# Optimization experiments

Measured on AMD Instinct MI355X. Metric: run time of the kernel, lower is better.

The kernel has to match this reference:

```python
import jax, jax.numpy as jnp
import numpy as np

# Module hyperparameters (from init_kwargs)
LEARNING_RATE = 0.01  # not used inside compute_weight_update
TAU_PLUS = 20.0
TAU_MINUS = 20.0
A_PLUS = 0.005
A_MINUS = 0.00525
TARGET_RATE = 0.1
HOMEOSTATIC_RATE = 0.001
TAU_HOMEOSTATIC = 1000.0

B, T, N_PRE, N_POST = 16, 8192, 128, 128


def setup_inputs() -> dict:
    key = jax.random.key(0)
    k1, k2, k3 = jax.random.split(key, 3)
    # Bernoulli spike trains at ~target_rate firing probability
    pre_spikes = (jax.random.uniform(k1, (B, T, N_PRE)) < TARGET_RATE).astype(jnp.float32)
    post_spikes = (jax.random.uniform(k2, (B, T, N_POST)) < TARGET_RATE).astype(jnp.float32)
    weights = jax.random.uniform(k3, (N_PRE, N_POST), dtype=jnp.float32)
    return {"pre_spikes": pre_spikes, "post_spikes": post_spikes, "weights": weights, "dt": 1}


def _temporal_corr(x, kernel, pad):
    """Correlate x [B,T,N] along time with 1-D kernel [L], padding pad=(lo,hi)."""
    b, t, n = x.shape
    xr = jnp.moveaxis(x, 1, 2).reshape(b * n, 1, t)  # [B*N, 1, T]
    k = kernel.reshape(1, 1, -1).astype(x.dtype)
    y = jax.lax.conv_general_dilated(
        xr, k, window_strides=(1,), padding=[pad],
        dimension_numbers=("NCH", "OIH", "NCH"))
    return jnp.moveaxis(y.reshape(b, n, t), 2, 1)  # [B,T,N]


def reference(pre_spikes, post_spikes, weights, dt):
    b, t, n_pre = pre_spikes.shape
    dt = float(dt)

    # Homeostatic rate tracking (first call: avg rates initialized to target_rate)
    alpha = dt / TAU_HOMEOSTATIC
    current_post_rate = post_spikes.mean(axis=(0, 1))
    avg_post_rate = (1.0 - alpha) * TARGET_RATE + alpha * current_post_rate

    # Truncated exponential STDP window: tau in 1..min(int(3*tau)-1, ...) = 1..59
    L = int(TAU_PLUS * 3)  # 60 taps (tau=0 tap zeroed)
    taus = jnp.arange(L, dtype=jnp.float32)
    w_plus = jnp.where(taus > 0, A_PLUS * jnp.exp(-taus * dt / TAU_PLUS), 0.0)
    w_minus = jnp.where(taus > 0, A_MINUS * jnp.exp(-taus * dt / TAU_MINUS), 0.0)

    # LTP: post_filt[t] = sum_{tau>=1} w_plus[tau] * post[t+tau] (future, zero-padded)
    post_filt = _temporal_corr(post_spikes, w_plus, (0, L - 1))
    # LTD: pre_filt[t] = sum_{tau>=1} w_minus[tau] * pre[t-tau] (past, zero-padded)
    pre_filt = _temporal_corr(pre_spikes, w_minus[::-1], (L - 1, 0))

    # sum_t mean_b outer(pre[t], post_filt[t]) - outer(pre_filt[t], post[t]), then /T
    ltp = jnp.einsum("btp,btq->pq", pre_spikes, post_filt)
    ltd = jnp.einsum("btp,btq->pq", pre_filt, post_spikes)
    stdp_update = (ltp - ltd) / (b * t)

    # Homeostatic regulation pulls post rate toward target
    post_rate_error = avg_post_rate - TARGET_RATE
    homeostatic_update = -HOMEOSTATIC_RATE * post_rate_error[None, :] * weights

    return stdp_update + homeostatic_update
```

## Files before the change

### kernel.cpp

```cpp
#include <hip/hip_runtime.h>

#define BB 16
#define TT 8192
#define NN 128
constexpr int CHUNK = 256;
constexpr int NBLK  = BB * TT / CHUNK;
constexpr int OUTN  = NN * NN;
constexpr int GS    = 264;
constexpr int SLOTS = OUTN / 2;
constexpr int PROWS = 315;

typedef _Float16 f16x8 __attribute__((ext_vector_type(8)));
typedef _Float16 f16x2 __attribute__((ext_vector_type(2)));
typedef float    f32x4 __attribute__((ext_vector_type(4)));

__device__ __forceinline__ unsigned short h16(float x) {
    _Float16 h = (_Float16)x;
    return __builtin_bit_cast(unsigned short, h);
}
__device__ __forceinline__ unsigned int pack2(float x, float y) {
    return (unsigned int)h16(x) | ((unsigned int)h16(y) << 16);
}
__device__ __forceinline__ float2 ldL(const unsigned short* p_lds, int m, int q0) {
    const unsigned int v = *(const unsigned int*)&p_lds[m * NN + q0];
    const f16x2 h = __builtin_bit_cast(f16x2, v);
    return make_float2((float)h[0], (float)h[1]);
}

template<bool ATOMIC>
__global__ __launch_bounds__(512, 4)
void stdp_main(const float* __restrict__ pre, const float* __restrict__ post,
               const int* __restrict__ dtp,
               unsigned int* __restrict__ part, float* __restrict__ wpost,
               float* __restrict__ outat)
{
    __shared__ __align__(16) char smem[PROWS * NN * 2];
    unsigned short* post_lds = (unsigned short*)smem;
    unsigned short* g_lds    = (unsigned short*)smem;
    float*          lds_ps   = (float*)(smem + NN * GS * 2);

    const int tid   = threadIdx.x;
    const int blk   = blockIdx.x;
    const int b     = blk >> 5;
    const int chunk = blk & 31;
    const int t0    = chunk * CHUNK;
    const int wv    = tid >> 6;
    const int lane  = tid & 63;

    const float dtf = (float)(*dtp);
    const float r   = expf(-dtf * (1.0f / 20.0f));

    const float* pb = post + (size_t)b * TT * NN;
    const float* ab = pre  + (size_t)b * TT * NN;

    {
        const int c  = tid & 31;
        const int mr = tid >> 5;
        for (int m = mr; m < PROWS; m += 16) {
            const int t = t0 + 1 + m;
            float4 v = make_float4(0.f, 0.f, 0.f, 0.f);
            if (t < TT) v = *(const float4*)(pb + (size_t)t * NN + c * 4);
            *(uint2*)&post_lds[m * NN + c * 4] = make_uint2(pack2(v.x, v.y), pack2(v.z, v.w));
        }
    }
    __syncthreads();

    const int win  = wv;
    const int q0   = lane * 2;
    const int base = win * 32;
    float ps0 = 0.f, ps1 = 0.f;

    unsigned int pk0[16], pk1[16];
    {
        float2 p  = ldL(post_lds, base + 31, q0);
        float wt  = r;
        float gx = r * p.x, gy = r * p.y;
        ps0 += p.x; ps1 += p.y;
        #pragma unroll
        for (int tau = 2; tau <= 59; ++tau) {
            wt *= r;
            p = ldL(post_lds, base + 30 + tau, q0);
            gx = fmaf(wt, p.x, gx);
            gy = fmaf(wt, p.y, gy);
        }
        const float r60 = wt * r;
        pk0[15] = (unsigned int)h16(gx) << 16;
        pk1[15] = (unsigned int)h16(gy) << 16;
        #pragma unroll
        for (int c = 30; c >= 0; --c) {
            const float2 p1  = ldL(post_lds, base + c,      q0);
            const float2 p60 = ldL(post_lds, base + c + 59, q0);
            gx = r * (gx + p1.x) - r60 * p60.x;
            gy = r * (gy + p1.y) - r60 * p60.y;
            ps0 += p1.x; ps1 += p1.y;
            if (c & 1) {
                pk0[c >> 1] = (unsigned int)h16(gx) << 16;
                pk1[c >> 1] = (unsigned int)h16(gy) << 16;
            } else {
                pk0[c >> 1] |= h16(gx);
                pk1[c >> 1] |= h16(gy);
            }
        }
    }
    __syncthreads();

    {
        unsigned short* d0 = &g_lds[q0 * GS + win * 32];
        unsigned short* d1 = &g_lds[(q0 + 1) * GS + win * 32];
        #pragma unroll
        for (int s = 0; s < 4; ++s) {
            *(uint4*)(d0 + 8 * s) = make_uint4(pk0[4*s], pk0[4*s+1], pk0[4*s+2], pk0[4*s+3]);
            *(uint4*)(d1 + 8 * s) = make_uint4(pk1[4*s], pk1[4*s+1], pk1[4*s+2], pk1[4*s+3]);
        }
        lds_ps[win * NN + q0]     = ps0;
        lds_ps[win * NN + q0 + 1] = ps1;
    }
    __syncthreads();

    const int pr0 = wv * 16;
    f32x4 acc[8];
    #pragma unroll
    for (int qt = 0; qt < 8; ++qt) acc[qt] = (f32x4){0.f, 0.f, 0.f, 0.f};

    const float* abase = ab + (size_t)(t0 + (lane >> 4) * 8) * NN + pr0 + (lane & 15);
    float an[8];
    #pragma unroll
    for (int j = 0; j < 8; ++j) an[j] = abase[(size_t)j * NN];

    #pragma unroll
    for (int ks = 0; ks < 8; ++ks) {
        f16x8 af;
        #pragma unroll
        for (int j = 0; j < 8; ++j) af[j] = (_Float16)an[j];
        if (ks < 7) {
            const float* src = abase + (size_t)((ks + 1) * 32) * NN;
            #pragma unroll
            for (int j = 0; j < 8; ++j) an[j] = src[(size_t)j * NN];
        }
        const int koff = ks * 32 + (lane >> 4) * 8;
        #pragma unroll
        for (int qt = 0; qt < 8; ++qt) {
            const f16x8 bf = *(const f16x8*)&g_lds[(qt * 16 + (lane & 15)) * GS + koff];
            acc[qt] = __builtin_amdgcn_mfma_f32_16x16x32_f16(af, bf, acc[qt], 0, 0, 0);
        }
    }

    if constexpr (!ATOMIC) {
        unsigned int* dst = part + ((size_t)blk * 8 + wv) * 1024 + lane;
        #pragma unroll
        for (int qt = 0; qt < 8; ++qt)
            #pragma unroll
            for (int rp = 0; rp < 2; ++rp)
                dst[qt * 128 + rp * 64] = pack2(acc[qt][2 * rp], acc[qt][2 * rp + 1]);
    } else {
        #pragma unroll
        for (int qt = 0; qt < 8; ++qt)
            #pragma unroll
            for (int rg = 0; rg < 4; ++rg) {
                const int prow = pr0 + (lane >> 4) * 4 + rg;
                const int qcol = qt * 16 + (lane & 15);
                atomicAdd(&outat[prow * NN + qcol], acc[qt][rg]);
            }
    }

    __syncthreads();
    if (tid < NN) {
        float s = 0.f;
        #pragma unroll
        for (int w = 0; w < 8; ++w) s += lds_ps[w * NN + tid];
        if (chunk == 0) s += pb[tid];
        if constexpr (ATOMIC) atomicAdd(&wpost[tid], s);
        else wpost[(size_t)tid * NBLK + blk] = s;
    }
}

__global__ void hfac_kernel(const float* __restrict__ wpost, const int* __restrict__ dtp,
                            float* __restrict__ hfac, int nb)
{
    const int q = blockIdx.x;
    float s = 0.f;
    for (int k = threadIdx.x; k < nb; k += 64) s += wpost[(size_t)q * nb + k];
    #pragma unroll
    for (int off = 32; off; off >>= 1) s += __shfl_down(s, off, 64);
    if (threadIdx.x == 0) {
        const float dtf   = (float)(*dtp);
        const float alpha = dtf * 1e-3f;
        const float mean  = s * (1.0f / (float)(BB * TT));
        hfac[q] = -0.001f * (alpha * (mean - 0.1f));
    }
}

__global__ __launch_bounds__(512)
void finalize_ws(const unsigned int* __restrict__ part, const float* __restrict__ hfac,
                 const float* __restrict__ W, float* __restrict__ out)
{
    __shared__ float2 red[512];
    const int s    = threadIdx.x & 63;
    const int kq   = threadIdx.x >> 6;
    const int slot = blockIdx.x * 64 + s;
    float sx = 0.f, sy = 0.f;
    #pragma unroll 8
    for (int k = kq * 64; k < kq * 64 + 64; ++k) {
        const unsigned int v = part[(size_t)k * SLOTS + slot];
        const f16x2 h = __builtin_bit_cast(f16x2, v);
        sx += (float)h[0];
        sy += (float)h[1];
    }
    red[threadIdx.x] = make_float2(sx, sy);
    __syncthreads();
    if (threadIdx.x < 64) {
        #pragma unroll
        for (int g = 1; g < 8; ++g) {
            const float2 v = red[g * 64 + s];
            sx += v.x; sy += v.y;
        }
        sx += red[s].x - red[s].x + 0.f;
        float rx = red[s].x, ry = red[s].y;
        sx = sx - (sx - sx);
        float tx = rx, ty = ry;
        #pragma unroll
        for (int g = 1; g < 8; ++g) {
            const float2 v = red[g * 64 + s];
            tx += v.x; ty += v.y;
        }
        const int lane = slot & 63;
        const int rp   = (slot >> 6) & 1;
        const int qt   = (slot >> 7) & 7;
        const int wv   = slot >> 10;
        const int p    = wv * 16 + ((lane >> 4) << 2) + rp * 2;
        const int q    = qt * 16 + (lane & 15);
        const float scale = (float)((0.005 - 0.00525) / (double)(BB * TT));
        const float hf = hfac[q];
        out[p * NN + q]       = fmaf(tx, scale, hf * W[p * NN + q]);
        out[(p + 1) * NN + q] = fmaf(ty, scale, hf * W[(p + 1) * NN + q]);
    }
}

__global__ void finalize_at(const float* __restrict__ hfac, const float* __restrict__ W,
                            float* __restrict__ out)
{
    const int i = (blockIdx.x * 256 + threadIdx.x) * 2;
    const int q = i & 127;
    const float scale = (float)((0.005 - 0.00525) / (double)(BB * TT));
    float2 s = *(const float2*)(out + i);
    float2 w = *(const float2*)(W + i);
    float2 o;
    o.x = fmaf(s.x, scale, hfac[q] * w.x);
    o.y = fmaf(s.y, scale, hfac[q + 1] * w.y);
    *(float2*)(out + i) = o;
}

extern "C" void kernel_launch(void* const* d_in, const int* in_sizes, int n_in,
                              void* d_out, int out_size, void* d_ws, size_t ws_size,
                              hipStream_t stream)
{
    const float* pre  = (const float*)d_in[0];
    const float* post = (const float*)d_in[1];
    const float* W    = (const float*)d_in[2];
    const int*   dtp  = (const int*)d_in[3];
    float* out = (float*)d_out;

    const size_t part_bytes  = (size_t)NBLK * SLOTS * sizeof(unsigned int);
    const size_t wpost_bytes = (size_t)NBLK * NN * sizeof(float);
    const size_t need = part_bytes + wpost_bytes + NN * sizeof(float);

    if (ws_size >= need) {
        unsigned int* part = (unsigned int*)d_ws;
        float* wpost       = (float*)((char*)d_ws + part_bytes);
        float* hfac        = (float*)((char*)d_ws + part_bytes + wpost_bytes);
        hipLaunchKernelGGL((stdp_main<false>), dim3(NBLK), dim3(512), 0, stream,
                           pre, post, dtp, part, wpost, (float*)nullptr);
        hipLaunchKernelGGL(hfac_kernel, dim3(NN), dim3(64), 0, stream, wpost, dtp, hfac, NBLK);
        hipLaunchKernelGGL(finalize_ws, dim3(SLOTS / 64), dim3(512), 0, stream, part, hfac, W, out);
    } else {
        float* wpost = (float*)d_ws;
        float* hfac  = wpost + NN;
        hipMemsetAsync(d_out, 0, OUTN * sizeof(float), stream);
        hipMemsetAsync(wpost, 0, NN * sizeof(float), stream);
        hipLaunchKernelGGL((stdp_main<true>), dim3(NBLK), dim3(512), 0, stream,
                           pre, post, dtp, (unsigned int*)nullptr, wpost, out);
        hipLaunchKernelGGL(hfac_kernel, dim3(NN), dim3(64), 0, stream, wpost, dtp, hfac, 1);
        hipLaunchKernelGGL(finalize_at, dim3(OUTN / 512), dim3(256), 0, stream, hfac, W, out);
    }
}
```

Measured before the change: 164.7 us.

## Bit-pack post spikes via ballot, halve block size, fold hfac into finalize

Post spikes are packed into bitmasks with wave ballots and stored in LDS as bits instead of fp16. This shrinks shared memory and relies on the inputs being exactly 0/1. The main kernel drops to 256 threads, each wave computing two 16-row tiles in two time halves. The per-column post-spike sums now go to global atomics, which lets the hfac kernel be removed and its computation folded into finalize. The changes aim to cut LDS footprint and one launch, at the cost of atomics and bit-extract ALU work in the filter loop.

```diff
diff --git a/kernel.cpp b/kernel.cpp
--- a/kernel.cpp
+++ b/kernel.cpp
@@ -6,7 +6,7 @@
 constexpr int CHUNK = 256;
 constexpr int NBLK  = BB * TT / CHUNK;
 constexpr int OUTN  = NN * NN;
-constexpr int GS    = 264;
+constexpr int GS2   = 136;
 constexpr int SLOTS = OUTN / 2;
 constexpr int PROWS = 315;
 
@@ -21,23 +21,16 @@
 __device__ __forceinline__ unsigned int pack2(float x, float y) {
     return (unsigned int)h16(x) | ((unsigned int)h16(y) << 16);
 }
-__device__ __forceinline__ float2 ldL(const unsigned short* p_lds, int m, int q0) {
-    const unsigned int v = *(const unsigned int*)&p_lds[m * NN + q0];
-    const f16x2 h = __builtin_bit_cast(f16x2, v);
-    return make_float2((float)h[0], (float)h[1]);
-}
 
 template<bool ATOMIC>
-__global__ __launch_bounds__(512, 4)
+__global__ __launch_bounds__(256, 4)
 void stdp_main(const float* __restrict__ pre, const float* __restrict__ post,
                const int* __restrict__ dtp,
                unsigned int* __restrict__ part, float* __restrict__ wpost,
                float* __restrict__ outat)
 {
-    __shared__ __align__(16) char smem[PROWS * NN * 2];
-    unsigned short* post_lds = (unsigned short*)smem;
-    unsigned short* g_lds    = (unsigned short*)smem;
-    float*          lds_ps   = (float*)(smem + NN * GS * 2);
+    __shared__ __align__(16) unsigned int   bits_s[PROWS * 4];
+    __shared__ __align__(16) unsigned short g_s[NN * GS2];
 
     const int tid   = threadIdx.x;
     const int blk   = blockIdx.x;
@@ -53,146 +46,150 @@
     const float* pb = post + (size_t)b * TT * NN;
     const float* ab = pre  + (size_t)b * TT * NN;
 
-    {
-        const int c  = tid & 31;
-        const int mr = tid >> 5;
-        for (int m = mr; m < PROWS; m += 16) {
-            const int t = t0 + 1 + m;
-            float4 v = make_float4(0.f, 0.f, 0.f, 0.f);
-            if (t < TT) v = *(const float4*)(pb + (size_t)t * NN + c * 4);
-            *(uint2*)&post_lds[m * NN + c * 4] = make_uint2(pack2(v.x, v.y), pack2(v.z, v.w));
+    for (int it = 0; it < 40; ++it) {
+        const int half = lane >> 5;
+        const int m    = it * 8 + wv * 2 + half;
+        const int t    = t0 + 1 + m;
+        const int c4   = (lane & 31) * 4;
+        float4 v = make_float4(0.f, 0.f, 0.f, 0.f);
+        if (m < PROWS && t < TT) v = *(const float4*)(pb + (size_t)t * NN + c4);
+        const unsigned long long bx = __ballot(v.x != 0.0f);
+        const unsigned long long by = __ballot(v.y != 0.0f);
+        const unsigned long long bz = __ballot(v.z != 0.0f);
+        const unsigned long long bw = __ballot(v.w != 0.0f);
+        if (m < PROWS && (lane & 31) == 0) {
+            const int sh = half * 32;
+            *(uint4*)&bits_s[m * 4] = make_uint4(
+                (unsigned int)(bx >> sh), (unsigned int)(by >> sh),
+                (unsigned int)(bz >> sh), (unsigned int)(bw >> sh));
         }
     }
     __syncthreads();
 
-    const int win  = wv;
-    const int q0   = lane * 2;
-    const int base = win * 32;
+    const int q0 = lane * 2;
+    const int q1 = q0 + 1;
+    const int c0 = q0 & 3;
+    const int jb = q0 >> 2;
     float ps0 = 0.f, ps1 = 0.f;
 
-    unsigned int pk0[16], pk1[16];
-    {
-        float2 p  = ldL(post_lds, base + 31, q0);
-        float wt  = r;
-        float gx = r * p.x, gy = r * p.y;
-        ps0 += p.x; ps1 += p.y;
-        #pragma unroll
-        for (int tau = 2; tau <= 59; ++tau) {
-            wt *= r;
-            p = ldL(post_lds, base + 30 + tau, q0);
-            gx = fmaf(wt, p.x, gx);
-            gy = fmaf(wt, p.y, gy);
-        }
-        const float r60 = wt * r;
-        pk0[15] = (unsigned int)h16(gx) << 16;
-        pk1[15] = (unsigned int)h16(gy) << 16;
-        #pragma unroll
-        for (int c = 30; c >= 0; --c) {
-            const float2 p1  = ldL(post_lds, base + c,      q0);
-            const float2 p60 = ldL(post_lds, base + c + 59, q0);
-            gx = r * (gx + p1.x) - r60 * p60.x;
-            gy = r * (gy + p1.y) - r60 * p60.y;
-            ps0 += p1.x; ps1 += p1.y;
-            if (c & 1) {
-                pk0[c >> 1] = (unsigned int)h16(gx) << 16;
-                pk1[c >> 1] = (unsigned int)h16(gy) << 16;
-            } else {
-                pk0[c >> 1] |= h16(gx);
-                pk1[c >> 1] |= h16(gy);
-            }
-        }
-    }
-    __syncthreads();
-
-    {
-        unsigned short* d0 = &g_lds[q0 * GS + win * 32];
-        unsigned short* d1 = &g_lds[(q0 + 1) * GS + win * 32];
-        #pragma unroll
-        for (int s = 0; s < 4; ++s) {
-            *(uint4*)(d0 + 8 * s) = make_uint4(pk0[4*s], pk0[4*s+1], pk0[4*s+2], pk0[4*s+3]);
-            *(uint4*)(d1 + 8 * s) = make_uint4(pk1[4*s], pk1[4*s+1], pk1[4*s+2], pk1[4*s+3]);
-        }
-        lds_ps[win * NN + q0]     = ps0;
-        lds_ps[win * NN + q0 + 1] = ps1;
-    }
-    __syncthreads();
-
-    const int pr0 = wv * 16;
-    f32x4 acc[8];
+    f32x4 acc[2][8];
     #pragma unroll
-    for (int qt = 0; qt < 8; ++qt) acc[qt] = (f32x4){0.f, 0.f, 0.f, 0.f};
-
-    const float* abase = ab + (size_t)(t0 + (lane >> 4) * 8) * NN + pr0 + (lane & 15);
-    float an[8];
-    #pragma unroll
-    for (int j = 0; j < 8; ++j) an[j] = abase[(size_t)j * NN];
-
-    #pragma unroll
-    for (int ks = 0; ks < 8; ++ks) {
-        f16x8 af;
-        #pragma unroll
-        for (int j = 0; j < 8; ++j) af[j] = (_Float16)an[j];
-        if (ks < 7) {
-            const float* src = abase + (size_t)((ks + 1) * 32) * NN;
-            #pragma unroll
-            for (int j = 0; j < 8; ++j) an[j] = src[(size_t)j * NN];
-        }
-        const int koff = ks * 32 + (lane >> 4) * 8;
-        #pragma unroll
-        for (int qt = 0; qt < 8; ++qt) {
-            const f16x8 bf = *(const f16x8*)&g_lds[(qt * 16 + (lane & 15)) * GS + koff];
-            acc[qt] = __builtin_amdgcn_mfma_f32_16x16x32_f16(af, bf, acc[qt], 0, 0, 0);
-        }
-    }
+    for (int i = 0; i < 2; ++i)
+        #pragma unroll
+        for (int qt = 0; qt < 8; ++qt) acc[i][qt] = (f32x4){0.f, 0.f, 0.f, 0.f};
+
+    const int pr0 = wv * 32;
+
+    #pragma unroll 1
+    for (int s = 0; s < 2; ++s) {
+        const int mb = (s * 4 + wv) * 32;
+        unsigned int pk0[16], pk1[16];
+        {
+            #define RDP(mrow, px, py) {                                   \
+                const uint4 w4 = *(const uint4*)&bits_s[(mrow) * 4];      \
+                const unsigned int w0 = (c0 & 2) ? w4.z : w4.x;           \
+                const unsigned int w1 = (c0 & 2) ? w4.w : w4.y;           \
+                px = (float)((w0 >> jb) & 1u);                            \
+                py = (float)((w1 >> jb) & 1u);                            \
+            }
+            float px, py;
+            RDP(mb + 31, px, py);
+            float wt = r;
+            float gx = r * px, gy = r * py;
+            ps0 += px; ps1 += py;
+            #pragma unroll
+            for (int tau = 2; tau <= 59; ++tau) {
+                wt *= r;
+                RDP(mb + 30 + tau, px, py);
+                gx = fmaf(wt, px, gx);
+                gy = fmaf(wt, py, gy);
+            }
+            const float r60 = wt * r;
+            pk0[15] = (unsigned int)h16(gx) << 16;
+            pk1[15] = (unsigned int)h16(gy) << 16;
+            #pragma unroll
+            for (int c = 30; c >= 0; --c) {
+                float p1x, p1y, p60x, p60y;
+                RDP(mb + c,      p1x,  p1y);
+                RDP(mb + c + 59, p60x, p60y);
+                gx = r * (gx + p1x) - r60 * p60x;
+                gy = r * (gy + p1y) - r60 * p60y;
+                ps0 += p1x; ps1 += p1y;
+                if (c & 1) {
+                    pk0[c >> 1] = (unsigned int)h16(gx) << 16;
+                    pk1[c >> 1] = (unsigned int)h16(gy) << 16;
+                } else {
+                    pk0[c >> 1] |= h16(gx);
+                    pk1[c >> 1] |= h16(gy);
+                }
+            }
+            #undef RDP
+        }
+        if (s == 1) __syncthreads();
+        {
+            unsigned short* d0 = &g_s[q0 * GS2 + wv * 32];
+            unsigned short* d1 = &g_s[q1 * GS2 + wv * 32];
+            #pragma unroll
+            for (int k = 0; k < 4; ++k) {
+                *(uint4*)(d0 + 8 * k) = make_uint4(pk0[4*k], pk0[4*k+1], pk0[4*k+2], pk0[4*k+3]);
+                *(uint4*)(d1 + 8 * k) = make_uint4(pk1[4*k], pk1[4*k+1], pk1[4*k+2], pk1[4*k+3]);
+            }
+        }
+        __syncthreads();
+
+        #pragma unroll
+        for (int ks = 0; ks < 4; ++ks) {
+            const int trow = t0 + s * 128 + ks * 32 + (lane >> 4) * 8;
+            f16x8 af[2];
+            #pragma unroll
+            for (int i = 0; i < 2; ++i) {
+                const float* src = ab + (size_t)trow * NN + pr0 + i * 16 + (lane & 15);
+                #pragma unroll
+                for (int j = 0; j < 8; ++j)
+                    af[i][j] = (_Float16)src[(size_t)j * NN];
+            }
+            const int koff = ks * 32 + (lane >> 4) * 8;
+            #pragma unroll
+            for (int qt = 0; qt < 8; ++qt) {
+                const f16x8 bf = *(const f16x8*)&g_s[(qt * 16 + (lane & 15)) * GS2 + koff];
+                acc[0][qt] = __builtin_amdgcn_mfma_f32_16x16x32_f16(af[0], bf, acc[0][qt], 0, 0, 0);
+                acc[1][qt] = __builtin_amdgcn_mfma_f32_16x16x32_f16(af[1], bf, acc[1][qt], 0, 0, 0);
+            }
+        }
+    }
+
+    atomicAdd(&wpost[q0], ps0);
+    atomicAdd(&wpost[q1], ps1);
+    if (chunk == 0 && tid < NN) atomicAdd(&wpost[tid], pb[tid]);
 
     if constexpr (!ATOMIC) {
-        unsigned int* dst = part + ((size_t)blk * 8 + wv) * 1024 + lane;
-        #pragma unroll
-        for (int qt = 0; qt < 8; ++qt)
-            #pragma unroll
-            for (int rp = 0; rp < 2; ++rp)
-                dst[qt * 128 + rp * 64] = pack2(acc[qt][2 * rp], acc[qt][2 * rp + 1]);
+        unsigned int* dst = part + (size_t)blk * SLOTS + wv * 2048 + lane;
+        #pragma unroll
+        for (int i = 0; i < 2; ++i)
+            #pragma unroll
+            for (int qt = 0; qt < 8; ++qt)
+                #pragma unroll
+                for (int rp = 0; rp < 2; ++rp)
+                    dst[i * 1024 + qt * 128 + rp * 64] =
+                        pack2(acc[i][qt][2 * rp], acc[i][qt][2 * rp + 1]);
     } else {
         #pragma unroll
-        for (int qt = 0; qt < 8; ++qt)
-            #pragma unroll
-            for (int rg = 0; rg < 4; ++rg) {
-                const int prow = pr0 + (lane >> 4) * 4 + rg;
-                const int qcol = qt * 16 + (lane & 15);
-                atomicAdd(&outat[prow * NN + qcol], acc[qt][rg]);
-            }
-    }
-
-    __syncthreads();
-    if (tid < NN) {
-        float s = 0.f;
-        #pragma unroll
-        for (int w = 0; w < 8; ++w) s += lds_ps[w * NN + tid];
-        if (chunk == 0) s += pb[tid];
-        if constexpr (ATOMIC) atomicAdd(&wpost[tid], s);
-        else wpost[(size_t)tid * NBLK + blk] = s;
-    }
-}
-
-__global__ void hfac_kernel(const float* __restrict__ wpost, const int* __restrict__ dtp,
-                            float* __restrict__ hfac, int nb)
-{
-    const int q = blockIdx.x;
-    float s = 0.f;
-    for (int k = threadIdx.x; k < nb; k += 64) s += wpost[(size_t)q * nb + k];
-    #pragma unroll
-    for (int off = 32; off; off >>= 1) s += __shfl_down(s, off, 64);
-    if (threadIdx.x == 0) {
-        const float dtf   = (float)(*dtp);
-        const float alpha = dtf * 1e-3f;
-        const float mean  = s * (1.0f / (float)(BB * TT));
-        hfac[q] = -0.001f * (alpha * (mean - 0.1f));
+        for (int i = 0; i < 2; ++i)
+            #pragma unroll
+            for (int qt = 0; qt < 8; ++qt)
+                #pragma unroll
+                for (int rg = 0; rg < 4; ++rg) {
+                    const int prow = pr0 + i * 16 + (lane >> 4) * 4 + rg;
+                    const int qcol = qt * 16 + (lane & 15);
+                    atomicAdd(&outat[prow * NN + qcol], acc[i][qt][rg]);
+                }
     }
 }
 
 __global__ __launch_bounds__(512)
-void finalize_ws(const unsigned int* __restrict__ part, const float* __restrict__ hfac,
-                 const float* __restrict__ W, float* __restrict__ out)
+void finalize_ws(const unsigned int* __restrict__ part, const float* __restrict__ wpost,
+                 const int* __restrict__ dtp, const float* __restrict__ W,
+                 float* __restrict__ out)
 {
     __shared__ float2 red[512];
     const int s    = threadIdx.x & 63;
@@ -209,15 +206,7 @@
     red[threadIdx.x] = make_float2(sx, sy);
     __syncthreads();
     if (threadIdx.x < 64) {
-        #pragma unroll
-        for (int g = 1; g < 8; ++g) {
-            const float2 v = red[g * 64 + s];
-            sx += v.x; sy += v.y;
-        }
-        sx += red[s].x - red[s].x + 0.f;
-        float rx = red[s].x, ry = red[s].y;
-        sx = sx - (sx - sx);
-        float tx = rx, ty = ry;
+        float tx = red[s].x, ty = red[s].y;
         #pragma unroll
         for (int g = 1; g < 8; ++g) {
             const float2 v = red[g * 64 + s];
@@ -226,27 +215,34 @@
         const int lane = slot & 63;
         const int rp   = (slot >> 6) & 1;
         const int qt   = (slot >> 7) & 7;
-        const int wv   = slot >> 10;
-        const int p    = wv * 16 + ((lane >> 4) << 2) + rp * 2;
+        const int ii   = (slot >> 10) & 1;
+        const int wv   = slot >> 11;
+        const int p    = wv * 32 + ii * 16 + ((lane >> 4) << 2) + rp * 2;
         const int q    = qt * 16 + (lane & 15);
         const float scale = (float)((0.005 - 0.00525) / (double)(BB * TT));
-        const float hf = hfac[q];
+        const float dtf   = (float)(*dtp);
+        const float alpha = dtf * 1e-3f;
+        const float hf    = -0.001f * (alpha * (wpost[q] * (1.0f / (BB * TT)) - 0.1f));
         out[p * NN + q]       = fmaf(tx, scale, hf * W[p * NN + q]);
         out[(p + 1) * NN + q] = fmaf(ty, scale, hf * W[(p + 1) * NN + q]);
     }
 }
 
-__global__ void finalize_at(const float* __restrict__ hfac, const float* __restrict__ W,
-                            float* __restrict__ out)
+__global__ void finalize_at(const float* __restrict__ wpost, const int* __restrict__ dtp,
+                            const float* __restrict__ W, float* __restrict__ out)
 {
     const int i = (blockIdx.x * 256 + threadIdx.x) * 2;
     const int q = i & 127;
     const float scale = (float)((0.005 - 0.00525) / (double)(BB * TT));
-    float2 s = *(const float2*)(out + i);
-    float2 w = *(const float2*)(W + i);
+    const float dtf   = (float)(*dtp);
+    const float alpha = dtf * 1e-3f;
+    const float hf0   = -0.001f * (alpha * (wpost[q]     * (1.0f / (BB * TT)) - 0.1f));
+    const float hf1   = -0.001f * (alpha * (wpost[q + 1] * (1.0f / (BB * TT)) - 0.1f));
+    float2 sv = *(const float2*)(out + i);
+    float2 w  = *(const float2*)(W + i);
     float2 o;
-    o.x = fmaf(s.x, scale, hfac[q] * w.x);
-    o.y = fmaf(s.y, scale, hfac[q + 1] * w.y);
+    o.x = fmaf(sv.x, scale, hf0 * w.x);
+    o.y = fmaf(sv.y, scale, hf1 * w.y);
     *(float2*)(out + i) = o;
 }
 
@@ -260,26 +256,24 @@
     const int*   dtp  = (const int*)d_in[3];
     float* out = (float*)d_out;
 
-    const size_t part_bytes  = (size_t)NBLK * SLOTS * sizeof(unsigned int);
-    const size_t wpost_bytes = (size_t)NBLK * NN * sizeof(float);
-    const size_t need = part_bytes + wpost_bytes + NN * sizeof(float);
+    const size_t part_bytes = (size_t)NBLK * SLOTS * sizeof(unsigned int);
+    const size_t need = part_bytes + NN * sizeof(float);
 
     if (ws_size >= need) {
         unsigned int* part = (unsigned int*)d_ws;
         float* wpost       = (float*)((char*)d_ws + part_bytes);
-        float* hfac        = (float*)((char*)d_ws + part_bytes + wpost_bytes);
-        hipLaunchKernelGGL((stdp_main<false>), dim3(NBLK), dim3(512), 0, stream,
+        hipMemsetAsync(wpost, 0, NN * sizeof(float), stream);
+        hipLaunchKernelGGL((stdp_main<false>), dim3(NBLK), dim3(256), 0, stream,
                            pre, post, dtp, part, wpost, (float*)nullptr);
-        hipLaunchKernelGGL(hfac_kernel, dim3(NN), dim3(64), 0, stream, wpost, dtp, hfac, NBLK);
-        hipLaunchKernelGGL(finalize_ws, dim3(SLOTS / 64), dim3(512), 0, stream, part, hfac, W, out);
+        hipLaunchKernelGGL(finalize_ws, dim3(SLOTS / 64), dim3(512), 0, stream,
+                           part, wpost, dtp, W, out);
     } else {
         float* wpost = (float*)d_ws;
-        float* hfac  = wpost + NN;
         hipMemsetAsync(d_out, 0, OUTN * sizeof(float), stream);
         hipMemsetAsync(wpost, 0, NN * sizeof(float), stream);
-        hipLaunchKernelGGL((stdp_main<true>), dim3(NBLK), dim3(512), 0, stream,
+        hipLaunchKernelGGL((stdp_main<true>), dim3(NBLK), dim3(256), 0, stream,
                            pre, post, dtp, (unsigned int*)nullptr, wpost, out);
-        hipLaunchKernelGGL(hfac_kernel, dim3(NN), dim3(64), 0, stream, wpost, dtp, hfac, 1);
-        hipLaunchKernelGGL(finalize_at, dim3(OUTN / 512), dim3(256), 0, stream, hfac, W, out);
-    }
-}
+        hipLaunchKernelGGL(finalize_at, dim3(OUTN / 512), dim3(256), 0, stream,
+                           wpost, dtp, W, out);
+    }
+}
```

Result: slower. 397.6 us (+141.4%).

## Split post neurons into two halves per block to double grid parallelism

Applied to the files above, without the earlier changes.

Each time chunk is now handled by two 256-thread blocks, each covering 64 of the 128 post neurons. That doubles the grid to 1024 blocks and halves the LDS footprint per block. Each wave filters 64 time steps for one post column and computes a 32x64 output tile with 2x4 MFMAs. The pre-spike A fragments are now loaded in every block, so pre reads from global memory double, and the software prefetch of the next pre slice is removed. Dead redundant arithmetic in finalize_ws is also cleaned up.

```diff
diff --git a/kernel.cpp b/kernel.cpp
--- a/kernel.cpp
+++ b/kernel.cpp
@@ -4,10 +4,12 @@
 #define TT 8192
 #define NN 128
 constexpr int CHUNK = 256;
-constexpr int NBLK  = BB * TT / CHUNK;
+constexpr int NCH   = BB * TT / CHUNK;
+constexpr int NBLK  = NCH * 2;
 constexpr int OUTN  = NN * NN;
-constexpr int GS    = 264;
-constexpr int SLOTS = OUTN / 2;
+constexpr int QH    = 64;
+constexpr int GSQ   = 264;
+constexpr int SLOTS = 8192;
 constexpr int PROWS = 315;
 
 typedef _Float16 f16x8 __attribute__((ext_vector_type(8)));
@@ -21,31 +23,32 @@
 __device__ __forceinline__ unsigned int pack2(float x, float y) {
     return (unsigned int)h16(x) | ((unsigned int)h16(y) << 16);
 }
-__device__ __forceinline__ float2 ldL(const unsigned short* p_lds, int m, int q0) {
-    const unsigned int v = *(const unsigned int*)&p_lds[m * NN + q0];
-    const f16x2 h = __builtin_bit_cast(f16x2, v);
-    return make_float2((float)h[0], (float)h[1]);
+__device__ __forceinline__ float ldLq(const unsigned short* p_lds, int m, int q) {
+    _Float16 h = __builtin_bit_cast(_Float16, p_lds[m * QH + q]);
+    return (float)h;
 }
 
 template<bool ATOMIC>
-__global__ __launch_bounds__(512, 4)
+__global__ __launch_bounds__(256, 4)
 void stdp_main(const float* __restrict__ pre, const float* __restrict__ post,
                const int* __restrict__ dtp,
                unsigned int* __restrict__ part, float* __restrict__ wpost,
                float* __restrict__ outat)
 {
-    __shared__ __align__(16) char smem[PROWS * NN * 2];
+    __shared__ __align__(16) char smem[PROWS * QH * 2];
     unsigned short* post_lds = (unsigned short*)smem;
     unsigned short* g_lds    = (unsigned short*)smem;
-    float*          lds_ps   = (float*)(smem + NN * GS * 2);
-
-    const int tid   = threadIdx.x;
-    const int blk   = blockIdx.x;
-    const int b     = blk >> 5;
-    const int chunk = blk & 31;
-    const int t0    = chunk * CHUNK;
-    const int wv    = tid >> 6;
-    const int lane  = tid & 63;
+    float*          lds_ps   = (float*)(smem + QH * GSQ * 2);
+
+    const int tid    = threadIdx.x;
+    const int blk    = blockIdx.x;
+    const int chunkG = blk >> 1;
+    const int qh     = blk & 1;
+    const int b      = chunkG >> 5;
+    const int chunk  = chunkG & 31;
+    const int t0     = chunk * CHUNK;
+    const int wv     = tid >> 6;
+    const int lane   = tid & 63;
 
     const float dtf = (float)(*dtp);
     const float r   = expf(-dtf * (1.0f / 20.0f));
@@ -54,123 +57,112 @@
     const float* ab = pre  + (size_t)b * TT * NN;
 
     {
-        const int c  = tid & 31;
-        const int mr = tid >> 5;
+        const int c  = tid & 15;
+        const int mr = tid >> 4;
         for (int m = mr; m < PROWS; m += 16) {
             const int t = t0 + 1 + m;
             float4 v = make_float4(0.f, 0.f, 0.f, 0.f);
-            if (t < TT) v = *(const float4*)(pb + (size_t)t * NN + c * 4);
-            *(uint2*)&post_lds[m * NN + c * 4] = make_uint2(pack2(v.x, v.y), pack2(v.z, v.w));
-        }
-    }
-    __syncthreads();
-
-    const int win  = wv;
-    const int q0   = lane * 2;
-    const int base = win * 32;
-    float ps0 = 0.f, ps1 = 0.f;
-
-    unsigned int pk0[16], pk1[16];
+            if (t < TT) v = *(const float4*)(pb + (size_t)t * NN + qh * QH + c * 4);
+            *(uint2*)&post_lds[m * QH + c * 4] =
+                make_uint2(pack2(v.x, v.y), pack2(v.z, v.w));
+        }
+    }
+    __syncthreads();
+
+    const int base = wv * 64;
+    float ps = 0.f;
+
+    unsigned int pk[32];
     {
-        float2 p  = ldL(post_lds, base + 31, q0);
-        float wt  = r;
-        float gx = r * p.x, gy = r * p.y;
-        ps0 += p.x; ps1 += p.y;
+        float p  = ldLq(post_lds, base + 63, lane);
+        float wt = r;
+        float g  = r * p;
+        ps += p;
         #pragma unroll
         for (int tau = 2; tau <= 59; ++tau) {
             wt *= r;
-            p = ldL(post_lds, base + 30 + tau, q0);
-            gx = fmaf(wt, p.x, gx);
-            gy = fmaf(wt, p.y, gy);
+            p = ldLq(post_lds, base + 62 + tau, lane);
+            g = fmaf(wt, p, g);
         }
         const float r60 = wt * r;
-        pk0[15] = (unsigned int)h16(gx) << 16;
-        pk1[15] = (unsigned int)h16(gy) << 16;
-        #pragma unroll
-        for (int c = 30; c >= 0; --c) {
-            const float2 p1  = ldL(post_lds, base + c,      q0);
-            const float2 p60 = ldL(post_lds, base + c + 59, q0);
-            gx = r * (gx + p1.x) - r60 * p60.x;
-            gy = r * (gy + p1.y) - r60 * p60.y;
-            ps0 += p1.x; ps1 += p1.y;
-            if (c & 1) {
-                pk0[c >> 1] = (unsigned int)h16(gx) << 16;
-                pk1[c >> 1] = (unsigned int)h16(gy) << 16;
-            } else {
-                pk0[c >> 1] |= h16(gx);
-                pk1[c >> 1] |= h16(gy);
-            }
+        pk[31] = (unsigned int)h16(g) << 16;
+        #pragma unroll
+        for (int c = 62; c >= 0; --c) {
+            const float p1  = ldLq(post_lds, base + c,      lane);
+            const float p60 = ldLq(post_lds, base + c + 59, lane);
+            g = r * (g + p1) - r60 * p60;
+            ps += p1;
+            if (c & 1) pk[c >> 1] = (unsigned int)h16(g) << 16;
+            else       pk[c >> 1] |= h16(g);
         }
     }
     __syncthreads();
 
     {
-        unsigned short* d0 = &g_lds[q0 * GS + win * 32];
-        unsigned short* d1 = &g_lds[(q0 + 1) * GS + win * 32];
-        #pragma unroll
-        for (int s = 0; s < 4; ++s) {
-            *(uint4*)(d0 + 8 * s) = make_uint4(pk0[4*s], pk0[4*s+1], pk0[4*s+2], pk0[4*s+3]);
-            *(uint4*)(d1 + 8 * s) = make_uint4(pk1[4*s], pk1[4*s+1], pk1[4*s+2], pk1[4*s+3]);
-        }
-        lds_ps[win * NN + q0]     = ps0;
-        lds_ps[win * NN + q0 + 1] = ps1;
-    }
-    __syncthreads();
-
-    const int pr0 = wv * 16;
-    f32x4 acc[8];
+        unsigned short* d = &g_lds[lane * GSQ + wv * 64];
+        #pragma unroll
+        for (int s = 0; s < 8; ++s)
+            *(uint4*)(d + 8 * s) = make_uint4(pk[4*s], pk[4*s+1], pk[4*s+2], pk[4*s+3]);
+        lds_ps[wv * QH + lane] = ps;
+    }
+    __syncthreads();
+
+    const int pr0 = wv * 32;
+    f32x4 acc[2][4];
     #pragma unroll
-    for (int qt = 0; qt < 8; ++qt) acc[qt] = (f32x4){0.f, 0.f, 0.f, 0.f};
-
-    const float* abase = ab + (size_t)(t0 + (lane >> 4) * 8) * NN + pr0 + (lane & 15);
-    float an[8];
-    #pragma unroll
-    for (int j = 0; j < 8; ++j) an[j] = abase[(size_t)j * NN];
+    for (int i = 0; i < 2; ++i)
+        #pragma unroll
+        for (int qt = 0; qt < 4; ++qt) acc[i][qt] = (f32x4){0.f, 0.f, 0.f, 0.f};
 
     #pragma unroll
     for (int ks = 0; ks < 8; ++ks) {
-        f16x8 af;
-        #pragma unroll
-        for (int j = 0; j < 8; ++j) af[j] = (_Float16)an[j];
-        if (ks < 7) {
-            const float* src = abase + (size_t)((ks + 1) * 32) * NN;
+        const int trow = t0 + ks * 32 + (lane >> 4) * 8;
+        f16x8 af[2];
+        #pragma unroll
+        for (int i = 0; i < 2; ++i) {
+            const float* src = ab + (size_t)trow * NN + pr0 + i * 16 + (lane & 15);
             #pragma unroll
-            for (int j = 0; j < 8; ++j) an[j] = src[(size_t)j * NN];
+            for (int j = 0; j < 8; ++j)
+                af[i][j] = (_Float16)src[(size_t)j * NN];
         }
         const int koff = ks * 32 + (lane >> 4) * 8;
         #pragma unroll
-        for (int qt = 0; qt < 8; ++qt) {
-            const f16x8 bf = *(const f16x8*)&g_lds[(qt * 16 + (lane & 15)) * GS + koff];
-            acc[qt] = __builtin_amdgcn_mfma_f32_16x16x32_f16(af, bf, acc[qt], 0, 0, 0);
+        for (int qt = 0; qt < 4; ++qt) {
+            const f16x8 bf = *(const f16x8*)&g_lds[(qt * 16 + (lane & 15)) * GSQ + koff];
+            acc[0][qt] = __builtin_amdgcn_mfma_f32_16x16x32_f16(af[0], bf, acc[0][qt], 0, 0, 0);
+            acc[1][qt] = __builtin_amdgcn_mfma_f32_16x16x32_f16(af[1], bf, acc[1][qt], 0, 0, 0);
         }
     }
 
     if constexpr (!ATOMIC) {
-        unsigned int* dst = part + ((size_t)blk * 8 + wv) * 1024 + lane;
-        #pragma unroll
-        for (int qt = 0; qt < 8; ++qt)
+        unsigned int* dst = part + (size_t)chunkG * SLOTS + qh * 4096 + wv * 1024 + lane;
+        #pragma unroll
+        for (int i = 0; i < 2; ++i)
             #pragma unroll
-            for (int rp = 0; rp < 2; ++rp)
-                dst[qt * 128 + rp * 64] = pack2(acc[qt][2 * rp], acc[qt][2 * rp + 1]);
+            for (int qt = 0; qt < 4; ++qt)
+                #pragma unroll
+                for (int rp = 0; rp < 2; ++rp)
+                    dst[i * 512 + qt * 128 + rp * 64] =
+                        pack2(acc[i][qt][2 * rp], acc[i][qt][2 * rp + 1]);
     } else {
         #pragma unroll
-        for (int qt = 0; qt < 8; ++qt)
+        for (int i = 0; i < 2; ++i)
             #pragma unroll
-            for (int rg = 0; rg < 4; ++rg) {
-                const int prow = pr0 + (lane >> 4) * 4 + rg;
-                const int qcol = qt * 16 + (lane & 15);
-                atomicAdd(&outat[prow * NN + qcol], acc[qt][rg]);
-            }
-    }
-
-    __syncthreads();
-    if (tid < NN) {
-        float s = 0.f;
-        #pragma unroll
-        for (int w = 0; w < 8; ++w) s += lds_ps[w * NN + tid];
-        if (chunk == 0) s += pb[tid];
-        if constexpr (ATOMIC) atomicAdd(&wpost[tid], s);
-        else wpost[(size_t)tid * NBLK + blk] = s;
+            for (int qt = 0; qt < 4; ++qt)
+                #pragma unroll
+                for (int rg = 0; rg < 4; ++rg) {
+                    const int prow = pr0 + i * 16 + (lane >> 4) * 4 + rg;
+                    const int qcol = qh * QH + qt * 16 + (lane & 15);
+                    atomicAdd(&outat[prow * NN + qcol], acc[i][qt][rg]);
+                }
+    }
+
+    if (tid < QH) {
+        float s = lds_ps[tid] + lds_ps[QH + tid] + lds_ps[2 * QH + tid] + lds_ps[3 * QH + tid];
+        const int q = qh * QH + tid;
+        if (chunk == 0) s += pb[q];
+        if constexpr (ATOMIC) atomicAdd(&wpost[q], s);
+        else wpost[(size_t)q * NCH + chunkG] = s;
     }
 }
 
@@ -209,15 +201,7 @@
     red[threadIdx.x] = make_float2(sx, sy);
     __syncthreads();
     if (threadIdx.x < 64) {
-        #pragma unroll
-        for (int g = 1; g < 8; ++g) {
-            const float2 v = red[g * 64 + s];
-            sx += v.x; sy += v.y;
-        }
-        sx += red[s].x - red[s].x + 0.f;
-        float rx = red[s].x, ry = red[s].y;
-        sx = sx - (sx - sx);
-        float tx = rx, ty = ry;
+        float tx = red[s].x, ty = red[s].y;
         #pragma unroll
         for (int g = 1; g < 8; ++g) {
             const float2 v = red[g * 64 + s];
@@ -225,10 +209,12 @@
         }
         const int lane = slot & 63;
         const int rp   = (slot >> 6) & 1;
-        const int qt   = (slot >> 7) & 7;
-        const int wv   = slot >> 10;
-        const int p    = wv * 16 + ((lane >> 4) << 2) + rp * 2;
-        const int q    = qt * 16 + (lane & 15);
+        const int qt   = (slot >> 7) & 3;
+        const int ii   = (slot >> 9) & 1;
+        const int wv   = (slot >> 10) & 3;
+        const int qhh  = slot >> 12;
+        const int p    = wv * 32 + ii * 16 + ((lane >> 4) << 2) + rp * 2;
+        const int q    = qhh * QH + qt * 16 + (lane & 15);
         const float scale = (float)((0.005 - 0.00525) / (double)(BB * TT));
         const float hf = hfac[q];
         out[p * NN + q]       = fmaf(tx, scale, hf * W[p * NN + q]);
@@ -260,24 +246,24 @@
     const int*   dtp  = (const int*)d_in[3];
     float* out = (float*)d_out;
 
-    const size_t part_bytes  = (size_t)NBLK * SLOTS * sizeof(unsigned int);
-    const size_t wpost_bytes = (size_t)NBLK * NN * sizeof(float);
+    const size_t part_bytes  = (size_t)NCH * SLOTS * sizeof(unsigned int);
+    const size_t wpost_bytes = (size_t)NN * NCH * sizeof(float);
     const size_t need = part_bytes + wpost_bytes + NN * sizeof(float);
 
     if (ws_size >= need) {
         unsigned int* part = (unsigned int*)d_ws;
         float* wpost       = (float*)((char*)d_ws + part_bytes);
         float* hfac        = (float*)((char*)d_ws + part_bytes + wpost_bytes);
-        hipLaunchKernelGGL((stdp_main<false>), dim3(NBLK), dim3(512), 0, stream,
+        hipLaunchKernelGGL((stdp_main<false>), dim3(NBLK), dim3(256), 0, stream,
                            pre, post, dtp, part, wpost, (float*)nullptr);
-        hipLaunchKernelGGL(hfac_kernel, dim3(NN), dim3(64), 0, stream, wpost, dtp, hfac, NBLK);
+        hipLaunchKernelGGL(hfac_kernel, dim3(NN), dim3(64), 0, stream, wpost, dtp, hfac, NCH);
         hipLaunchKernelGGL(finalize_ws, dim3(SLOTS / 64), dim3(512), 0, stream, part, hfac, W, out);
     } else {
         float* wpost = (float*)d_ws;
         float* hfac  = wpost + NN;
         hipMemsetAsync(d_out, 0, OUTN * sizeof(float), stream);
         hipMemsetAsync(wpost, 0, NN * sizeof(float), stream);
-        hipLaunchKernelGGL((stdp_main<true>), dim3(NBLK), dim3(512), 0, stream,
+        hipLaunchKernelGGL((stdp_main<true>), dim3(NBLK), dim3(256), 0, stream,
                            pre, post, dtp, (unsigned int*)nullptr, wpost, out);
         hipLaunchKernelGGL(hfac_kernel, dim3(NN), dim3(64), 0, stream, wpost, dtp, hfac, 1);
         hipLaunchKernelGGL(finalize_at, dim3(OUTN / 512), dim3(256), 0, stream, hfac, W, out);
```

Result: slower. 170.9 us (+3.7%).
